# Kernel tuning notes

Hardware: AMD Instinct MI355X
Metric: run time of the kernel (lower is better)

The kernel has to match this reference:

```python
import jax, jax.numpy as jnp
import numpy as np

# LLRDenoiser config (init_kwargs): ndim=2, patch W=8, stride S=4, ths=0.1, rand_shift=False
P = 8      # patch size (isotropic)
STRIDE = 4 # patch stride
THS = 0.1  # soft-threshold on singular values
B, C, H, W = 2, 16, 512, 512  # batch, coefficient axis, spatial dims


def setup_inputs() -> dict:
    key = jax.random.key(0)
    x = jax.random.normal(key, (B, C, H, W), dtype=jnp.float32)
    return {"x": x}


def _patch_idx(n, p, s):
    # start indices for sliding windows, inclusive of last full window
    starts = jnp.arange(0, n - p + 1, s)
    return starts[:, None] + jnp.arange(p)[None, :]  # (n_patches, p)


def _llr_denoise(x):
    idx_h = _patch_idx(H, P, STRIDE)  # (nH, P)
    idx_w = _patch_idx(W, P, STRIDE)  # (nW, P)
    nH, nW = idx_h.shape[0], idx_w.shape[0]
    hi = idx_h[:, None, :, None]  # (nH, 1, P, 1)
    wi = idx_w[None, :, None, :]  # (1, nW, 1, P)

    # extract overlapping patches -> (B, C, nH, nW, P, P)
    patches = x[:, :, hi, wi]
    # Casorati matrices per patch: (B, nH*nW, C, P*P)
    mats = patches.transpose(0, 2, 3, 1, 4, 5).reshape(B, nH * nW, C, P * P)

    # batched thin SVD + soft-threshold of singular values
    u, s, vh = jnp.linalg.svd(mats, full_matrices=False)
    s_st = jnp.sign(s) * jnp.maximum(jnp.abs(s) - THS, 0.0)
    mats = (u * s_st[..., None, :]) @ vh

    # back to patch layout (B, C, nH, nW, P, P)
    patches = mats.reshape(B, nH, nW, C, P, P).transpose(0, 3, 1, 2, 4, 5)

    # overlap-add reconstruction, averaged by patch coverage count
    out = jnp.zeros_like(x).at[:, :, hi, wi].add(patches)
    cnt = jnp.zeros((H, W), x.dtype).at[hi[..., 0, :, :] if False else idx_h[:, None, :, None], idx_w[None, :, None, :]].add(1.0)
    return out / cnt


def reference(x):
    return _llr_denoise(x)
```

## Files before the change

kernel.cpp:

```cpp
#include <hip/hip_runtime.h>


#define NBATCH  2
#define NCH     16
#define HDIM    512
#define WDIM    512
#define NPH     127
#define NPW     127
#define NPATCH  (NBATCH * NPH * NPW)
#define NCELL   128
#define THS     0.1f
#define NSIT    7

typedef short bf16x8 __attribute__((ext_vector_type(8)));
typedef float f32x4  __attribute__((ext_vector_type(4)));

#define MFMA(a,b,c) __builtin_amdgcn_mfma_f32_16x16x32_bf16((a),(b),(c),0,0,0)

static __device__ inline short f2bf(float x) {
  return __builtin_bit_cast(short, (__bf16)x);
}
static __device__ inline float blo2f(unsigned int v) {
  return __builtin_bit_cast(float, v << 16);
}
static __device__ inline float bhi2f(unsigned int v) {
  return __builtin_bit_cast(float, v & 0xffff0000u);
}
static __device__ inline unsigned int pack2bf(float lo, float hi) {
  unsigned int a = (unsigned short)f2bf(lo);
  unsigned int b = (unsigned short)f2bf(hi);
  return (b << 16) | a;
}

static __device__ inline int xcd_swz(int b, int nwg) {
  const int q = nwg >> 3, r = nwg & 7;
  const int x = b & 7, lo = b >> 3;
  return (x < r ? x * (q + 1) : r * (q + 1) + (x - r) * q) + lo;
}

static __device__ inline bf16x8 fragc(f32x4 v) {
  bf16x8 r;
  r[0] = f2bf(v[0]); r[1] = f2bf(v[1]); r[2] = f2bf(v[2]); r[3] = f2bf(v[3]);
  r[4] = 0; r[5] = 0; r[6] = 0; r[7] = 0;
  return r;
}

#define ZS_NBLK ((NPATCH + 3) / 4)
__global__ __launch_bounds__(256) void llr_zs(const float* __restrict__ x,
                                              uint2* __restrict__ zs) {
  const int blk = xcd_swz(blockIdx.x, ZS_NBLK);
  const int pid = blk * 4 + (threadIdx.x >> 6);
  if (pid >= NPATCH) return;
  const int bi  = pid / (NPH * NPW);
  const int pr  = pid % (NPH * NPW);
  const int ph  = pr / NPW, pw = pr % NPW;
  const int h0  = ph * 4, w0 = pw * 4;
  const int l   = threadIdx.x & 63;
  const int j   = l & 15;
  const int u   = l >> 4;

  const size_t HW = (size_t)HDIM * WDIM;
  const float* xb = x + (size_t)bi * NCH * HW;

  const float* pb = xb + (size_t)j * HW + (size_t)h0 * WDIM + w0;
  const int dh0 = (u >> 1), dw0 = 4 * (u & 1);
  float4 q0 = *(const float4*)(pb + (size_t)(dh0 + 0) * WDIM + dw0);
  float4 q1 = *(const float4*)(pb + (size_t)(dh0 + 2) * WDIM + dw0);
  float4 q2 = *(const float4*)(pb + (size_t)(dh0 + 4) * WDIM + dw0);
  float4 q3 = *(const float4*)(pb + (size_t)(dh0 + 6) * WDIM + dw0);

  bf16x8 m0, m1;
  m0[0]=f2bf(q0.x); m0[1]=f2bf(q0.y); m0[2]=f2bf(q0.z); m0[3]=f2bf(q0.w);
  m0[4]=f2bf(q1.x); m0[5]=f2bf(q1.y); m0[6]=f2bf(q1.z); m0[7]=f2bf(q1.w);
  m1[0]=f2bf(q2.x); m1[1]=f2bf(q2.y); m1[2]=f2bf(q2.z); m1[3]=f2bf(q2.w);
  m1[4]=f2bf(q3.x); m1[5]=f2bf(q3.y); m1[6]=f2bf(q3.z); m1[7]=f2bf(q3.w);

  f32x4 g = {0.f, 0.f, 0.f, 0.f};
  g = MFMA(m0, m0, g);
  g = MFMA(m1, m1, g);

  float s2 = g[0]*g[0] + g[1]*g[1] + g[2]*g[2] + g[3]*g[3];
  #pragma unroll
  for (int m = 32; m >= 1; m >>= 1) s2 += __shfl_xor(s2, m, 64);

  uint2 wv = {0u, 0u};
  if (s2 > 1e-20f) {
    const float invf  = rsqrtf(s2);
    const float gsc   = 2.0f * invf;
    const float alpha = THS * sqrtf(gsc);

    f32x4 Yc, Zc;
    #pragma unroll
    for (int r = 0; r < 4; ++r) {
      Yc[r] = g[r] * gsc;
      Zc[r] = (4 * u + r == j) ? 1.0f : 0.0f;
    }

    const f32x4 zero = {0.f, 0.f, 0.f, 0.f};
    for (int it = 0; it < NSIT - 1; ++it) {
      bf16x8 yF = fragc(Yc), zF = fragc(Zc);
      f32x4 t  = MFMA(zF, yF, zero);
      bf16x8 tF = fragc(t);
      f32x4 py = MFMA(yF, tF, zero);
      f32x4 pz = MFMA(tF, zF, zero);
      #pragma unroll
      for (int r = 0; r < 4; ++r) {
        Yc[r] = 1.5f * Yc[r] - 0.5f * py[r];
        Zc[r] = 1.5f * Zc[r] - 0.5f * pz[r];
      }
    }
    {
      bf16x8 yF = fragc(Yc), zF = fragc(Zc);
      f32x4 t  = MFMA(zF, yF, zero);
      bf16x8 tF = fragc(t);
      f32x4 pz = MFMA(tF, zF, zero);
      #pragma unroll
      for (int r = 0; r < 4; ++r) Zc[r] = 1.5f * Zc[r] - 0.5f * pz[r];
    }

    wv.x = pack2bf(alpha * Zc[0], alpha * Zc[1]);
    wv.y = pack2bf(alpha * Zc[2], alpha * Zc[3]);
  }
  zs[(size_t)pid * 64 + l] = wv;
}

#define Q_NBLK (NBATCH * NCELL * 4)
__global__ __launch_bounds__(512, 8) void llr_q(const float* __restrict__ x,
                                                const uint2* __restrict__ zs,
                                                float* __restrict__ out) {
  __shared__ float RS[33 * 260];

  const int bid = blockIdx.x;
  const int qs  = bid & 3;
  const int ci  = (bid >> 2) & 127;
  const int bi  = bid >> 9;
  const int t   = threadIdx.x;
  const int r   = t >> 7;
  const int px  = t & 127;
  const int c   = px >> 2;

  const size_t HW = (size_t)HDIM * WDIM;
  const int h   = 4 * ci + r;
  const int wpx = qs * 128 + px;

  {
    const int w8 = t >> 6;
    const int l  = t & 63;
    const int u  = l >> 4, j = l & 15;
    const uint2* zb = zs + (size_t)bi * NPH * NPW * 64;
    const bool vh0 = (ci > 0), vh1 = (ci < NPH);
    const int ph0c = vh0 ? ci - 1 : 0;
    const int ph1c = vh1 ? ci : NPH - 1;
    for (int s = w8; s < 33; s += 8) {
      const int pw = qs * 32 - 1 + s;
      const bool vw = ((unsigned)pw <= (unsigned)(NPW - 1));
      const int pwc = vw ? pw : 0;
      uint2 z0 = zb[((size_t)ph0c * NPW + pwc) * 64 + l];
      uint2 z1 = zb[((size_t)ph1c * NPW + pwc) * 64 + l];
      if (!(vw && vh0)) { z0.x = 0u; z0.y = 0u; }
      if (!(vw && vh1)) { z1.x = 0u; z1.y = 0u; }
      float* rs = &RS[s * 260 + j];
      rs[16 * (4 * u + 0)] = blo2f(z0.x) + blo2f(z1.x);
      rs[16 * (4 * u + 1)] = bhi2f(z0.x) + bhi2f(z1.x);
      rs[16 * (4 * u + 2)] = blo2f(z0.y) + blo2f(z1.y);
      rs[16 * (4 * u + 3)] = bhi2f(z0.y) + bhi2f(z1.y);
    }
  }
  __syncthreads();

  const float* xp = x + (size_t)bi * NCH * HW + (size_t)h * WDIM + wpx;
  float xv[16];
  #pragma unroll
  for (int e = 0; e < 16; ++e) xv[e] = xp[(size_t)e * HW];

  const int cj = qs * 32 + c;
  const float cnth = 2.0f - (ci == 0) - (ci == NCELL - 1);
  const float cntw = 2.0f - (cj == 0) - (cj == NCELL - 1);
  const float sc = 1.0f / (cnth * cntw);

  const float* rsA = &RS[c * 260];
  const float* rsB = &RS[(c + 1) * 260];
  float* po = out + (size_t)bi * NCH * HW + (size_t)h * WDIM + wpx;
  #pragma unroll
  for (int co = 0; co < 16; ++co) {
    float acc = 0.f;
    #pragma unroll
    for (int k = 0; k < 4; ++k) {
      const float4 A = *(const float4*)(rsA + 16 * co + 4 * k);
      const float4 B = *(const float4*)(rsB + 16 * co + 4 * k);
      acc += (A.x + B.x) * xv[4 * k + 0];
      acc += (A.y + B.y) * xv[4 * k + 1];
      acc += (A.z + B.z) * xv[4 * k + 2];
      acc += (A.w + B.w) * xv[4 * k + 3];
    }
    po[(size_t)co * HW] = xv[co] - sc * acc;
  }
}

extern "C" void kernel_launch(void* const* d_in, const int* in_sizes, int n_in,
                              void* d_out, int out_size, void* d_ws, size_t ws_size,
                              hipStream_t stream) {
  const float* x = (const float*)d_in[0];
  float* out = (float*)d_out;
  uint2* zs = (uint2*)d_ws;

  llr_zs<<<dim3(ZS_NBLK), dim3(256), 0, stream>>>(x, zs);
  llr_q<<<dim3(Q_NBLK), dim3(512), 0, stream>>>(x, zs, out);
}
```

Measured before the change: 47.04 us.

## Restructure apply kernel into double-buffered two-chunk pipeline and cut Newton-Schulz iterations

The apply kernel now uses 256-thread blocks, and each block walks two 64-column chunks. Per-cell weight matrices are built in LDS as the four-patch sum with the coverage scale already folded in, and the global loads for the second chunk are issued before the first chunk's matvec runs. This removes the per-pixel A+B addition and the scale multiply, and overlaps zs loads with compute. Separately, the Newton-Schulz iteration count drops from 7 to 6, which reduces MFMA work in the first kernel but may loosen the accuracy of the inverse square root.

```diff
diff --git a/kernel.cpp b/kernel.cpp
--- a/kernel.cpp
+++ b/kernel.cpp
@@ -10,7 +10,7 @@
 #define NPATCH  (NBATCH * NPH * NPW)
 #define NCELL   128
 #define THS     0.1f
-#define NSIT    7
+#define NSIT    6
 
 typedef short bf16x8 __attribute__((ext_vector_type(8)));
 typedef float f32x4  __attribute__((ext_vector_type(4)));
@@ -125,76 +125,111 @@
 }
 
 #define Q_NBLK (NBATCH * NCELL * 4)
-__global__ __launch_bounds__(512, 8) void llr_q(const float* __restrict__ x,
-                                                const uint2* __restrict__ zs,
-                                                float* __restrict__ out) {
-  __shared__ float RS[33 * 260];
+__global__ __launch_bounds__(256, 4) void llr_ap(const float* __restrict__ x,
+                                                 const uint2* __restrict__ zs,
+                                                 float* __restrict__ out) {
+  __shared__ float PWf[2][16 * 260];
 
   const int bid = blockIdx.x;
-  const int qs  = bid & 3;
+  const int q   = bid & 3;
   const int ci  = (bid >> 2) & 127;
   const int bi  = bid >> 9;
   const int t   = threadIdx.x;
-  const int r   = t >> 7;
-  const int px  = t & 127;
+  const int r   = t >> 6;
+  const int px  = t & 63;
   const int c   = px >> 2;
 
   const size_t HW = (size_t)HDIM * WDIM;
-  const int h   = 4 * ci + r;
-  const int wpx = qs * 128 + px;
-
-  {
-    const int w8 = t >> 6;
-    const int l  = t & 63;
-    const int u  = l >> 4, j = l & 15;
-    const uint2* zb = zs + (size_t)bi * NPH * NPW * 64;
-    const bool vh0 = (ci > 0), vh1 = (ci < NPH);
-    const int ph0c = vh0 ? ci - 1 : 0;
-    const int ph1c = vh1 ? ci : NPH - 1;
-    for (int s = w8; s < 33; s += 8) {
-      const int pw = qs * 32 - 1 + s;
-      const bool vw = ((unsigned)pw <= (unsigned)(NPW - 1));
-      const int pwc = vw ? pw : 0;
-      uint2 z0 = zb[((size_t)ph0c * NPW + pwc) * 64 + l];
-      uint2 z1 = zb[((size_t)ph1c * NPW + pwc) * 64 + l];
-      if (!(vw && vh0)) { z0.x = 0u; z0.y = 0u; }
-      if (!(vw && vh1)) { z1.x = 0u; z1.y = 0u; }
-      float* rs = &RS[s * 260 + j];
-      rs[16 * (4 * u + 0)] = blo2f(z0.x) + blo2f(z1.x);
-      rs[16 * (4 * u + 1)] = bhi2f(z0.x) + bhi2f(z1.x);
-      rs[16 * (4 * u + 2)] = blo2f(z0.y) + blo2f(z1.y);
-      rs[16 * (4 * u + 3)] = bhi2f(z0.y) + bhi2f(z1.y);
-    }
-  }
+  const int h  = 4 * ci + r;
+  const int w4 = t >> 6;
+  const int l  = t & 63;
+  const int u  = l >> 4, j = l & 15;
+
+  const uint2* zb = zs + (size_t)bi * NPH * NPW * 64;
+  const bool vh0 = (ci > 0), vh1 = (ci < NPH);
+  const int ph0c = vh0 ? ci - 1 : 0;
+  const int ph1c = vh1 ? ci : NPH - 1;
+  const float cnth = 2.0f - (ci == 0) - (ci == NCELL - 1);
+
+  uint2 zr[4][4];
+
+#define GLOAD(OC)                                                           \
+  do {                                                                      \
+    _Pragma("unroll")                                                       \
+    for (int rd = 0; rd < 4; ++rd) {                                        \
+      const int cj  = (OC) * 16 + rd * 4 + w4;                              \
+      const int pwlc = (cj - 1 >= 0) ? cj - 1 : 0;                          \
+      const int pwrc = (cj <= NPW - 1) ? cj : NPW - 1;                      \
+      zr[rd][0] = zb[((size_t)ph0c * NPW + pwlc) * 64 + l];                 \
+      zr[rd][1] = zb[((size_t)ph0c * NPW + pwrc) * 64 + l];                 \
+      zr[rd][2] = zb[((size_t)ph1c * NPW + pwlc) * 64 + l];                 \
+      zr[rd][3] = zb[((size_t)ph1c * NPW + pwrc) * 64 + l];                 \
+    }                                                                       \
+  } while (0)
+
+#define GSTORE(OC, BUF)                                                     \
+  do {                                                                      \
+    _Pragma("unroll")                                                       \
+    for (int rd = 0; rd < 4; ++rd) {                                        \
+      const int cc = rd * 4 + w4;                                           \
+      const int cj = (OC) * 16 + cc;                                        \
+      const bool vl = (cj - 1 >= 0), vr = (cj <= NPW - 1);                  \
+      uint2 z00 = zr[rd][0], z01 = zr[rd][1];                               \
+      uint2 z10 = zr[rd][2], z11 = zr[rd][3];                               \
+      if (!(vh0 && vl)) { z00.x = 0u; z00.y = 0u; }                         \
+      if (!(vh0 && vr)) { z01.x = 0u; z01.y = 0u; }                         \
+      if (!(vh1 && vl)) { z10.x = 0u; z10.y = 0u; }                         \
+      if (!(vh1 && vr)) { z11.x = 0u; z11.y = 0u; }                         \
+      const float cntw = 2.0f - (cj == 0) - (cj == NCELL - 1);              \
+      const float sc = 1.0f / (cnth * cntw);                                \
+      float* wb = &PWf[BUF][cc * 260 + j];                                  \
+      wb[16 * (4 * u + 0)] = sc * (blo2f(z00.x) + blo2f(z01.x) + blo2f(z10.x) + blo2f(z11.x)); \
+      wb[16 * (4 * u + 1)] = sc * (bhi2f(z00.x) + bhi2f(z01.x) + bhi2f(z10.x) + bhi2f(z11.x)); \
+      wb[16 * (4 * u + 2)] = sc * (blo2f(z00.y) + blo2f(z01.y) + blo2f(z10.y) + blo2f(z11.y)); \
+      wb[16 * (4 * u + 3)] = sc * (bhi2f(z00.y) + bhi2f(z01.y) + bhi2f(z10.y) + bhi2f(z11.y)); \
+    }                                                                       \
+  } while (0)
+
+#define MATVEC(OC, BUF)                                                     \
+  do {                                                                      \
+    const int wpx = (OC) * 64 + px;                                         \
+    const float* xp = x + (size_t)bi * NCH * HW + (size_t)h * WDIM + wpx;   \
+    float xv[16];                                                           \
+    _Pragma("unroll")                                                       \
+    for (int e = 0; e < 16; ++e) xv[e] = xp[(size_t)e * HW];                \
+    const float* wb = &PWf[BUF][c * 260];                                   \
+    float* po = out + (size_t)bi * NCH * HW + (size_t)h * WDIM + wpx;       \
+    _Pragma("unroll")                                                       \
+    for (int co = 0; co < 16; ++co) {                                       \
+      float acc = 0.f;                                                      \
+      _Pragma("unroll")                                                     \
+      for (int k = 0; k < 4; ++k) {                                         \
+        const float4 W4 = *(const float4*)(wb + 16 * co + 4 * k);           \
+        acc += W4.x * xv[4 * k + 0];                                        \
+        acc += W4.y * xv[4 * k + 1];                                        \
+        acc += W4.z * xv[4 * k + 2];                                        \
+        acc += W4.w * xv[4 * k + 3];                                        \
+      }                                                                     \
+      po[(size_t)co * HW] = xv[co] - acc;                                   \
+    }                                                                       \
+  } while (0)
+
+  const int oc0 = 2 * q, oc1 = 2 * q + 1;
+
+  GLOAD(oc0);
+  GSTORE(oc0, 0);
   __syncthreads();
 
-  const float* xp = x + (size_t)bi * NCH * HW + (size_t)h * WDIM + wpx;
-  float xv[16];
-  #pragma unroll
-  for (int e = 0; e < 16; ++e) xv[e] = xp[(size_t)e * HW];
-
-  const int cj = qs * 32 + c;
-  const float cnth = 2.0f - (ci == 0) - (ci == NCELL - 1);
-  const float cntw = 2.0f - (cj == 0) - (cj == NCELL - 1);
-  const float sc = 1.0f / (cnth * cntw);
-
-  const float* rsA = &RS[c * 260];
-  const float* rsB = &RS[(c + 1) * 260];
-  float* po = out + (size_t)bi * NCH * HW + (size_t)h * WDIM + wpx;
-  #pragma unroll
-  for (int co = 0; co < 16; ++co) {
-    float acc = 0.f;
-    #pragma unroll
-    for (int k = 0; k < 4; ++k) {
-      const float4 A = *(const float4*)(rsA + 16 * co + 4 * k);
-      const float4 B = *(const float4*)(rsB + 16 * co + 4 * k);
-      acc += (A.x + B.x) * xv[4 * k + 0];
-      acc += (A.y + B.y) * xv[4 * k + 1];
-      acc += (A.z + B.z) * xv[4 * k + 2];
-      acc += (A.w + B.w) * xv[4 * k + 3];
-    }
-    po[(size_t)co * HW] = xv[co] - sc * acc;
-  }
+  GLOAD(oc1);
+  MATVEC(oc0, 0);
+  GSTORE(oc1, 1);
+  __syncthreads();
+
+  MATVEC(oc1, 1);
+
+#undef GLOAD
+#undef GSTORE
+#undef MATVEC
 }
 
 extern "C" void kernel_launch(void* const* d_in, const int* in_sizes, int n_in,
@@ -205,5 +240,5 @@
   uint2* zs = (uint2*)d_ws;
 
   llr_zs<<<dim3(ZS_NBLK), dim3(256), 0, stream>>>(x, zs);
-  llr_q<<<dim3(Q_NBLK), dim3(512), 0, stream>>>(x, zs, out);
-}
+  llr_ap<<<dim3(Q_NBLK), dim3(256), 0, stream>>>(x, zs, out);
+}
```

Result: faster. 42.54 us (-9.6%).
